# Performance work log

Measured on AMD Instinct MI355X. Metric: run time of the kernel, lower is better.

Reference implementation:

```python
import jax, jax.numpy as jnp
import numpy as np

B, S, HID = 2, 2048, 2048
NH = 16
HD = HID // NH  # 128


def setup_inputs() -> dict:
    key = jax.random.key(0)
    ks = jax.random.split(key, 9)
    w = 0.02  # init scale to keep logits in a sane range
    return {
        "hidden_states": jax.random.normal(ks[0], (B, S, HID), dtype=jnp.float32),
        "Wq": jax.random.normal(ks[1], (HID, HID), dtype=jnp.float32) * w,
        "bq": jnp.zeros((HID,), dtype=jnp.float32),
        "Wk": jax.random.normal(ks[2], (HID, HD), dtype=jnp.float32) * w,
        "bk": jnp.zeros((HD,), dtype=jnp.float32),
        "Wv": jax.random.normal(ks[3], (HID, HD), dtype=jnp.float32) * w,
        "bv": jnp.zeros((HD,), dtype=jnp.float32),
        "Wo": jax.random.normal(ks[4], (HID, HID), dtype=jnp.float32) * w,
        "bo": jnp.zeros((HID,), dtype=jnp.float32),
    }


def reference(hidden_states, Wq, bq, Wk, bk, Wv, bv, Wo, bo):
    b, s, _ = hidden_states.shape
    # Projections (weights stored [in, out])
    q = hidden_states @ Wq + bq                      # [B,S,HID]
    k = hidden_states @ Wk + bk                      # [B,S,HD] single shared KV head
    v = hidden_states @ Wv + bv                      # [B,S,HD]
    q = q.reshape(b, s, NH, HD)                      # [B,S,H,D]
    # MQA: all query heads attend to the same K/V
    scores = jnp.einsum("bshd,btd->bhst", q, k) / jnp.sqrt(jnp.float32(HD))  # [B,H,S,S]
    probs = jax.nn.softmax(scores, axis=-1)
    attn = jnp.einsum("bhst,btd->bshd", probs, v)    # [B,S,H,D]
    attn = attn.reshape(b, s, HID)
    return attn @ Wo + bo
```

## Files before the change

### kernel.cpp

```cpp
#include <hip/hip_runtime.h>
#include <math.h>

#define BB  2
#define SS  2048
#define HID 2048
#define NH  16
#define HD  128
#define MT  (BB * SS)
#define NC  (HID + 2 * HD)
#define QK_SCALE 0.12751744f

typedef unsigned short ushort_t;
typedef unsigned int uint_t;
typedef __bf16 bf16x8 __attribute__((ext_vector_type(8)));
typedef short short8 __attribute__((ext_vector_type(8)));
typedef float f32x4 __attribute__((ext_vector_type(4)));

__device__ __forceinline__ ushort_t f2bf(float x) {
    union { float f; uint_t u; } a; a.f = x;
    return (ushort_t)((a.u + 0x7FFFu + ((a.u >> 16) & 1u)) >> 16);
}
__device__ __forceinline__ ushort_t f2bf_fast(float x) {
    union { float f; uint_t u; } a; a.f = x;
    return (ushort_t)((a.u + 0x8000u) >> 16);
}

__device__ __forceinline__ int sw_addr(int r, int c) {
    return ((r >> 1) << 6) + ((((((r & 1) << 2) | c)) ^ ((r >> 1) & 7)) << 3);
}

#define CFENCE() asm volatile("" ::: "memory")

__global__ __launch_bounds__(256) void conv_bf16_kernel(
    const float* __restrict__ in, ushort_t* __restrict__ outb)
{
    const size_t i = ((size_t)blockIdx.x * 256 + threadIdx.x) * 8;
    const float4 a = *(const float4*)&in[i];
    const float4 b = *(const float4*)&in[i + 4];
    short8 o;
    o[0] = (short)f2bf(a.x); o[1] = (short)f2bf(a.y);
    o[2] = (short)f2bf(a.z); o[3] = (short)f2bf(a.w);
    o[4] = (short)f2bf(b.x); o[5] = (short)f2bf(b.y);
    o[6] = (short)f2bf(b.z); o[7] = (short)f2bf(b.w);
    *(short8*)&outb[i] = o;
}

__global__ __launch_bounds__(256) void convT_kernel(
    const float* __restrict__ W, ushort_t* __restrict__ Th, int K, int N)
{
    __shared__ float Ts[64][65];
    const int t = threadIdx.x;
    const int k0 = blockIdx.x * 64, n0 = blockIdx.y * 64;
    const int rr = t >> 4, c4 = (t & 15) * 4;
#pragma unroll
    for (int i = 0; i < 4; i++) {
        const int k = rr + i * 16;
        const float4 v = *(const float4*)&W[(size_t)(k0 + k) * N + n0 + c4];
        Ts[k][c4 + 0] = v.x; Ts[k][c4 + 1] = v.y;
        Ts[k][c4 + 2] = v.z; Ts[k][c4 + 3] = v.w;
    }
    __syncthreads();
    const int n = t >> 2, kc = (t & 3) * 16;
    short8 hv[2];
#pragma unroll
    for (int jj = 0; jj < 16; jj++)
        hv[jj >> 3][jj & 7] = (short)f2bf(Ts[kc + jj][n]);
    const size_t ob = (size_t)(n0 + n) * K + k0 + kc;
    *(short8*)&Th[ob]     = hv[0];
    *(short8*)&Th[ob + 8] = hv[1];
}

template<int GX, int MODE>
__global__ __launch_bounds__(512, 2) void gemm256_kernel(
    const ushort_t* __restrict__ Ab, const ushort_t* __restrict__ WT,
    const float* __restrict__ bqp, const float* __restrict__ bkp,
    const float* __restrict__ bvp,
    ushort_t* __restrict__ qb, ushort_t* __restrict__ kb,
    ushort_t* __restrict__ vtb, float* __restrict__ Cf)
{
    __shared__ short lds[32768];
    constexpr int K = HID;
    const int t = threadIdx.x;
    const int w = t >> 6, ln = t & 63;
    const int wm = w >> 2, wn = w & 3;
    const int nh = wn >> 1;
    const int q = ln >> 4, lm = ln & 15;

    const int nwg = GX * (MT / 256);
    const int bid = blockIdx.x;
    const int sw = (bid & 7) * (nwg >> 3) + (bid >> 3);
    const int bx = sw % GX, by = sw / GX;
    const int row0 = by * 256, col0 = bx * 256;

    const int lrow = w * 8 + (ln >> 3);
    const int sb = (ln & 7) ^ (lrow & 7);
    const int rs = lrow * 2 + (sb >> 2);
    const int cc = sb & 3;
    size_t agb[2], bgb[2];
    agb[0] = (size_t)(row0 + rs) * K + cc * 8;
    agb[1] = (size_t)(row0 + 128 + rs) * K + cc * 8;
    bgb[0] = (size_t)(col0 + rs) * K + cc * 8;
    bgb[1] = (size_t)(col0 + 128 + rs) * K + cc * 8;
    const int lseg = w * 512;

    int aofl[8], bofl[4];
#pragma unroll
    for (int mf = 0; mf < 8; mf++) aofl[mf] = sw_addr(mf * 16 + lm, q);
#pragma unroll
    for (int nf = 0; nf < 4; nf++) bofl[nf] = sw_addr((wn & 1) * 64 + nf * 16 + lm, q);

#define ACH(bufv, hv) ((((bufv) << 1) | (hv)) << 12)
#define STAGE_A(bufv, hv, kcol) \
    __builtin_amdgcn_global_load_lds( \
        (const __attribute__((address_space(1))) void*)(Ab + agb[hv] + (kcol)), \
        (__attribute__((address_space(3))) void*)&lds[ACH(bufv, hv) + lseg], 16, 0, 0)
#define STAGE_B(bufv, hv, kcol) \
    __builtin_amdgcn_global_load_lds( \
        (const __attribute__((address_space(1))) void*)(WT + bgb[hv] + (kcol)), \
        (__attribute__((address_space(3))) void*)&lds[16384 + ACH(bufv, hv) + lseg], 16, 0, 0)

    f32x4 acc[8][4];
#pragma unroll
    for (int i = 0; i < 8; i++)
#pragma unroll
        for (int j = 0; j < 4; j++) acc[i][j] = 0.f;

    STAGE_A(0, 0, 0); STAGE_A(0, 1, 0);
    STAGE_B(0, 0, 0); STAGE_B(0, 1, 0);

    for (int kt = 0; kt < K; kt += 32) {
        const int cur = (kt >> 5) & 1, nxt = cur ^ 1;
        const bool more = (kt + 32 < K);

        if (more) {
            STAGE_A(nxt, 0, kt + 32); STAGE_A(nxt, 1, kt + 32);
            STAGE_B(nxt, 0, kt + 32); STAGE_B(nxt, 1, kt + 32);
            asm volatile("s_waitcnt vmcnt(4)" ::: "memory");
        } else {
            asm volatile("s_waitcnt vmcnt(0)" ::: "memory");
        }
        CFENCE(); __builtin_amdgcn_s_barrier(); CFENCE();

        bf16x8 ah[8], bh[4];
#pragma unroll
        for (int mf = 0; mf < 8; mf++)
            ah[mf] = *(const bf16x8*)&lds[ACH(cur, wm) + aofl[mf]];
#pragma unroll
        for (int nf = 0; nf < 4; nf++)
            bh[nf] = *(const bf16x8*)&lds[16384 + ACH(cur, nh) + bofl[nf]];

        __builtin_amdgcn_s_setprio(1);
#pragma unroll
        for (int mf = 0; mf < 8; mf++)
#pragma unroll
            for (int nf = 0; nf < 4; nf++)
                acc[mf][nf] = __builtin_amdgcn_mfma_f32_16x16x32_bf16(
                    ah[mf], bh[nf], acc[mf][nf], 0, 0, 0);
        __builtin_amdgcn_s_setprio(0);

        CFENCE(); __builtin_amdgcn_s_barrier(); CFENCE();
    }
#undef STAGE_A
#undef STAGE_B
#undef ACH

#pragma unroll
    for (int nf = 0; nf < 4; nf++) {
        const int nnb = col0 + wn * 64 + nf * 16;
        const int nn = nnb + lm;
        if (MODE == 1) {
            const float bj = bqp[nn];
#pragma unroll
            for (int mf = 0; mf < 8; mf++) {
                const int mb = row0 + wm * 128 + mf * 16 + q * 4;
#pragma unroll
                for (int r = 0; r < 4; r++)
                    Cf[(size_t)(mb + r) * HID + nn] = acc[mf][nf][r] + bj;
            }
        } else {
            const int mode = (nnb < HID) ? 0 : ((nnb < HID + HD) ? 1 : 2);
            const float bj = (mode == 0) ? bqp[nn]
                           : (mode == 1) ? bkp[nn - HID] : bvp[nn - HID - HD];
#pragma unroll
            for (int mf = 0; mf < 8; mf++) {
                const int mb = row0 + wm * 128 + mf * 16 + q * 4;
#pragma unroll
                for (int r = 0; r < 4; r++) {
                    const float v = acc[mf][nf][r] + bj;
                    if (mode == 0)
                        qb[(size_t)(mb + r) * HID + nn] = f2bf_fast(v * QK_SCALE);
                    else if (mode == 1)
                        kb[(size_t)(mb + r) * HD + (nn - HID)] = f2bf_fast(v);
                    else
                        vtb[(size_t)(nn - HID - HD) * MT + (mb + r)] = f2bf_fast(v);
                }
            }
        }
    }
}

__global__ __launch_bounds__(128, 2) void attn_mfma_kernel(
    const ushort_t* __restrict__ qg, const ushort_t* __restrict__ kg,
    const ushort_t* __restrict__ vtg, ushort_t* Oh)
{
    __shared__ short Ks[8192], Vts[8192], Ps[4096];
    const int b = blockIdx.z, h = blockIdx.y, qt = blockIdx.x;
    const int t = threadIdx.x, wv = t >> 6, ln = t & 63;
    const int q = ln >> 4, lm = ln & 15;
    const int w32 = wv * 32;
    const int lm7 = ln & 7;

    const ushort_t* qgb = qg + (size_t)(b * SS + qt * 64) * HID + h * HD;
#pragma unroll
    for (int i = 0; i < 8; i++) {
        const int I = wv * 8 + i;
        const int r = 4 * I + (ln >> 4);
        const int c = (ln & 15) ^ (r & 15);
        __builtin_amdgcn_global_load_lds(
            (const __attribute__((address_space(1))) void*)(qgb + (size_t)r * HID + c * 8),
            (__attribute__((address_space(3))) void*)&Ks[I * 512], 16, 0, 0);
    }
    __syncthreads();
    bf16x8 aq[2][4];
#pragma unroll
    for (int st = 0; st < 2; st++) {
        const int am = w32 + st * 16 + lm;
#pragma unroll
        for (int ks = 0; ks < 4; ks++)
            aq[st][ks] = *(const bf16x8*)&Ks[am * 128 + (((ks << 2) | q) ^ (am & 15)) * 8];
    }
    __syncthreads();

    const ushort_t* kgb = kg + (size_t)b * SS * HD;
    const ushort_t* vgb = vtg + b * SS;
    uint_t koff[8], voff[8];
#pragma unroll
    for (int i = 0; i < 8; i++) {
        const int I = wv * 8 + i;
        { const int r = 4 * I + (ln >> 4); const int c = (ln & 15) ^ (r & 15);
          koff[i] = (uint_t)(r * HD + c * 8); }
        { const int r = 8 * I + (ln >> 3); const int c = (ln & 7) ^ (r & 7);
          voff[i] = (uint_t)(r * MT + c * 8); }
    }

#pragma unroll
    for (int i = 0; i < 8; i++) {
        const int I = wv * 8 + i;
        __builtin_amdgcn_global_load_lds(
            (const __attribute__((address_space(1))) void*)(kgb + koff[i]),
            (__attribute__((address_space(3))) void*)&Ks[I * 512], 16, 0, 0);
    }
#pragma unroll
    for (int i = 0; i < 8; i++) {
        const int I = wv * 8 + i;
        __builtin_amdgcn_global_load_lds(
            (const __attribute__((address_space(1))) void*)(vgb + voff[i]),
            (__attribute__((address_space(3))) void*)&Vts[I * 512], 16, 0, 0);
    }

    float lrow[2][4] = {{0.f, 0.f, 0.f, 0.f}, {0.f, 0.f, 0.f, 0.f}};
    f32x4 O[2][8];
#pragma unroll
    for (int st = 0; st < 2; st++)
#pragma unroll
        for (int ct = 0; ct < 8; ct++) O[st][ct] = 0.f;

    for (int kt = 0; kt < SS; kt += 64) {
        const int more = (kt + 64 < SS);

        asm volatile("s_waitcnt vmcnt(8)" ::: "memory");
        CFENCE();
        __builtin_amdgcn_s_barrier();
        CFENCE();

        f32x4 s[2][4];
#pragma unroll
        for (int st = 0; st < 2; st++)
#pragma unroll
            for (int ct = 0; ct < 4; ct++) s[st][ct] = 0.f;
        __builtin_amdgcn_s_setprio(1);
#pragma unroll
        for (int ks = 0; ks < 4; ks++) {
#pragma unroll
            for (int ct = 0; ct < 4; ct++) {
                const int n = ct * 16 + lm;
                const bf16x8 bk = *(const bf16x8*)&Ks[n * 128 + (((ks << 2) | q) ^ (n & 15)) * 8];
                s[0][ct] = __builtin_amdgcn_mfma_f32_16x16x32_bf16(aq[0][ks], bk, s[0][ct], 0, 0, 0);
                s[1][ct] = __builtin_amdgcn_mfma_f32_16x16x32_bf16(aq[1][ks], bk, s[1][ct], 0, 0, 0);
            }
        }
        __builtin_amdgcn_s_setprio(0);

        CFENCE();
        __builtin_amdgcn_s_barrier();
        CFENCE();
        if (more) {
#pragma unroll
            for (int i = 0; i < 8; i++) {
                const int I = wv * 8 + i;
                __builtin_amdgcn_global_load_lds(
                    (const __attribute__((address_space(1))) void*)(kgb + koff[i] + (kt + 64) * HD),
                    (__attribute__((address_space(3))) void*)&Ks[I * 512], 16, 0, 0);
            }
        }

#pragma unroll
        for (int st = 0; st < 2; st++)
#pragma unroll
        for (int ct = 0; ct < 4; ct++) {
            const int ch = ct * 2 + (lm >> 3);
#pragma unroll
            for (int r = 0; r < 4; r++) {
                const float p = exp2f(s[st][ct][r]);
                lrow[st][r] += p;
                const int pr = w32 + st * 16 + q * 4 + r;
                Ps[pr * 64 + ((ch ^ (pr & 7)) << 3) + lm7] = (short)f2bf_fast(p);
            }
        }

        if (more) asm volatile("s_waitcnt vmcnt(8)" ::: "memory");
        else      asm volatile("s_waitcnt vmcnt(0)" ::: "memory");
        CFENCE();
        __builtin_amdgcn_s_barrier();
        CFENCE();

        __builtin_amdgcn_s_setprio(1);
#pragma unroll
        for (int ks = 0; ks < 2; ks++) {
            const bf16x8 ap0 = *(const bf16x8*)&Ps[(w32 + lm) * 64 + (((ks << 2) | q) ^ lm7) * 8];
            const bf16x8 ap1 = *(const bf16x8*)&Ps[(w32 + 16 + lm) * 64 + (((ks << 2) | q) ^ lm7) * 8];
#pragma unroll
            for (int ct = 0; ct < 8; ct++) {
                const int d = ct * 16 + lm;
                const bf16x8 bv = *(const bf16x8*)&Vts[d * 64 + (((ks << 2) | q) ^ (d & 7)) * 8];
                O[0][ct] = __builtin_amdgcn_mfma_f32_16x16x32_bf16(ap0, bv, O[0][ct], 0, 0, 0);
                O[1][ct] = __builtin_amdgcn_mfma_f32_16x16x32_bf16(ap1, bv, O[1][ct], 0, 0, 0);
            }
        }
        __builtin_amdgcn_s_setprio(0);

        CFENCE();
        __builtin_amdgcn_s_barrier();
        CFENCE();
        if (more) {
#pragma unroll
            for (int i = 0; i < 8; i++) {
                const int I = wv * 8 + i;
                __builtin_amdgcn_global_load_lds(
                    (const __attribute__((address_space(1))) void*)(vgb + voff[i] + (kt + 64)),
                    (__attribute__((address_space(3))) void*)&Vts[I * 512], 16, 0, 0);
            }
        }
    }

#pragma unroll
    for (int msk = 1; msk < 16; msk <<= 1)
#pragma unroll
        for (int st = 0; st < 2; st++)
#pragma unroll
            for (int r = 0; r < 4; r++) lrow[st][r] += __shfl_xor(lrow[st][r], msk);
#pragma unroll
    for (int st = 0; st < 2; st++)
#pragma unroll
    for (int r = 0; r < 4; r++) {
        const float inv = 1.f / lrow[st][r];
        const size_t base = (size_t)(b * SS + qt * 64 + w32 + st * 16 + q * 4 + r) * HID + h * HD;
#pragma unroll
        for (int ct = 0; ct < 8; ct++)
            Oh[base + ct * 16 + lm] = f2bf_fast(O[st][ct][r] * inv);
    }
}

extern "C" void kernel_launch(void* const* d_in, const int* in_sizes, int n_in,
                              void* d_out, int out_size, void* d_ws, size_t ws_size,
                              hipStream_t stream)
{
    const float* hs = (const float*)d_in[0];
    const float* Wq = (const float*)d_in[1];
    const float* bq = (const float*)d_in[2];
    const float* Wk = (const float*)d_in[3];
    const float* bk = (const float*)d_in[4];
    const float* Wv = (const float*)d_in[5];
    const float* bv = (const float*)d_in[6];
    const float* Wo = (const float*)d_in[7];
    const float* bo = (const float*)d_in[8];
    float* out = (float*)d_out;

    char* w = (char*)d_ws;
    ushort_t* hsb  = (ushort_t*)w;  w += (size_t)MT * HID * 2;
    ushort_t* qb   = (ushort_t*)w;  w += (size_t)MT * HID * 2;
    ushort_t* kb   = (ushort_t*)w;  w += (size_t)MT * HD * 2;
    ushort_t* vtb  = (ushort_t*)w;  w += (size_t)HD * MT * 2;
    ushort_t* WcT  = (ushort_t*)w;  w += (size_t)NC * HID * 2;
    ushort_t* WoT  = WcT;

    conv_bf16_kernel<<<(MT * HID) / (256 * 8), 256, 0, stream>>>(hs, hsb);
    convT_kernel<<<dim3(HID / 64, HID / 64), 256, 0, stream>>>(Wq, WcT, HID, HID);
    convT_kernel<<<dim3(HID / 64, HD / 64),  256, 0, stream>>>(
        Wk, WcT + (size_t)HID * HID, HID, HD);
    convT_kernel<<<dim3(HID / 64, HD / 64),  256, 0, stream>>>(
        Wv, WcT + (size_t)(HID + HD) * HID, HID, HD);

    gemm256_kernel<NC / 256, 0><<<(NC / 256) * (MT / 256), 512, 0, stream>>>(
        hsb, WcT, bq, bk, bv, qb, kb, vtb, nullptr);

    convT_kernel<<<dim3(HID / 64, HID / 64), 256, 0, stream>>>(Wo, WoT, HID, HID);

    attn_mfma_kernel<<<dim3(SS / 64, NH, BB), 128, 0, stream>>>(qb, kb, vtb, qb);

    gemm256_kernel<HID / 256, 1><<<(HID / 256) * (MT / 256), 512, 0, stream>>>(
        qb, WoT, bo, nullptr, nullptr, nullptr, nullptr, nullptr, out);
}
```

Measured before the change: 359.5 us.

## Deepen GEMM K-step to 64 with interleaved staged loads across four MFMA phases

The projection GEMM kernel now processes K in 64-wide steps, doubling LDS to 128KB. Each step is split into four MFMA quadrant phases, and the next tile's global-to-LDS loads are issued chunk by chunk between them so copies overlap compute with fewer full waits per K. The attention softmax also swaps exp2f for the hardware exp2 builtin. Risks: the larger LDS footprint likely caps occupancy at one workgroup per CU despite launch_bounds(512,2), and there are more barriers per iteration.

```diff
diff --git a/kernel.cpp b/kernel.cpp
--- a/kernel.cpp
+++ b/kernel.cpp
@@ -78,7 +78,7 @@
     ushort_t* __restrict__ qb, ushort_t* __restrict__ kb,
     ushort_t* __restrict__ vtb, float* __restrict__ Cf)
 {
-    __shared__ short lds[32768];
+    __shared__ short lds[65536];
     constexpr int K = HID;
     const int t = threadIdx.x;
     const int w = t >> 6, ln = t & 63;
@@ -109,15 +109,15 @@
 #pragma unroll
     for (int nf = 0; nf < 4; nf++) bofl[nf] = sw_addr((wn & 1) * 64 + nf * 16 + lm, q);
 
-#define ACH(bufv, hv) ((((bufv) << 1) | (hv)) << 12)
-#define STAGE_A(bufv, hv, kcol) \
+#define CHUNK(bufv, hv, kcv) ((((bufv) << 2) | ((hv) << 1) | (kcv)) << 12)
+#define STAGE_A(bufv, hv, kcv, kcol) \
     __builtin_amdgcn_global_load_lds( \
-        (const __attribute__((address_space(1))) void*)(Ab + agb[hv] + (kcol)), \
-        (__attribute__((address_space(3))) void*)&lds[ACH(bufv, hv) + lseg], 16, 0, 0)
-#define STAGE_B(bufv, hv, kcol) \
+        (const __attribute__((address_space(1))) void*)(Ab + agb[hv] + (kcol) + (kcv) * 32), \
+        (__attribute__((address_space(3))) void*)&lds[CHUNK(bufv, hv, kcv) + lseg], 16, 0, 0)
+#define STAGE_B(bufv, hv, kcv, kcol) \
     __builtin_amdgcn_global_load_lds( \
-        (const __attribute__((address_space(1))) void*)(WT + bgb[hv] + (kcol)), \
-        (__attribute__((address_space(3))) void*)&lds[16384 + ACH(bufv, hv) + lseg], 16, 0, 0)
+        (const __attribute__((address_space(1))) void*)(WT + bgb[hv] + (kcol) + (kcv) * 32), \
+        (__attribute__((address_space(3))) void*)&lds[32768 + CHUNK(bufv, hv, kcv) + lseg], 16, 0, 0)
 
     f32x4 acc[8][4];
 #pragma unroll
@@ -125,44 +125,101 @@
 #pragma unroll
         for (int j = 0; j < 4; j++) acc[i][j] = 0.f;
 
-    STAGE_A(0, 0, 0); STAGE_A(0, 1, 0);
-    STAGE_B(0, 0, 0); STAGE_B(0, 1, 0);
-
-    for (int kt = 0; kt < K; kt += 32) {
-        const int cur = (kt >> 5) & 1, nxt = cur ^ 1;
-        const bool more = (kt + 32 < K);
+    STAGE_A(0, 0, 0, 0); STAGE_B(0, 0, 0, 0);
+    STAGE_A(0, 0, 1, 0); STAGE_B(0, 0, 1, 0);
+    STAGE_A(0, 1, 0, 0); STAGE_B(0, 1, 0, 0);
+    STAGE_A(0, 1, 1, 0); STAGE_B(0, 1, 1, 0);
+
+    for (int kt = 0; kt < K; kt += 64) {
+        const int cur = (kt >> 6) & 1, nxt = cur ^ 1;
+        const bool more = (kt + 64 < K);
+        const int kn = kt + 64;
+        bf16x8 ah[4][2], bh[4][2];
 
         if (more) {
-            STAGE_A(nxt, 0, kt + 32); STAGE_A(nxt, 1, kt + 32);
-            STAGE_B(nxt, 0, kt + 32); STAGE_B(nxt, 1, kt + 32);
-            asm volatile("s_waitcnt vmcnt(4)" ::: "memory");
+            STAGE_A(nxt, 0, 0, kn); STAGE_B(nxt, 0, 0, kn);
+            asm volatile("s_waitcnt vmcnt(2)" ::: "memory");
         } else {
             asm volatile("s_waitcnt vmcnt(0)" ::: "memory");
         }
         CFENCE(); __builtin_amdgcn_s_barrier(); CFENCE();
-
-        bf16x8 ah[8], bh[4];
-#pragma unroll
-        for (int mf = 0; mf < 8; mf++)
-            ah[mf] = *(const bf16x8*)&lds[ACH(cur, wm) + aofl[mf]];
-#pragma unroll
-        for (int nf = 0; nf < 4; nf++)
-            bh[nf] = *(const bf16x8*)&lds[16384 + ACH(cur, nh) + bofl[nf]];
-
-        __builtin_amdgcn_s_setprio(1);
-#pragma unroll
-        for (int mf = 0; mf < 8; mf++)
-#pragma unroll
-            for (int nf = 0; nf < 4; nf++)
-                acc[mf][nf] = __builtin_amdgcn_mfma_f32_16x16x32_bf16(
-                    ah[mf], bh[nf], acc[mf][nf], 0, 0, 0);
-        __builtin_amdgcn_s_setprio(0);
-
+#pragma unroll
+        for (int mfl = 0; mfl < 4; mfl++)
+#pragma unroll
+            for (int ks = 0; ks < 2; ks++)
+                ah[mfl][ks] = *(const bf16x8*)&lds[CHUNK(cur, wm, ks) + aofl[mfl]];
+#pragma unroll
+        for (int nfl = 0; nfl < 2; nfl++)
+#pragma unroll
+            for (int ks = 0; ks < 2; ks++)
+                bh[nfl][ks] = *(const bf16x8*)&lds[32768 + CHUNK(cur, nh, ks) + bofl[nfl]];
+        __builtin_amdgcn_s_setprio(1);
+#pragma unroll
+        for (int ks = 0; ks < 2; ks++)
+#pragma unroll
+            for (int mfl = 0; mfl < 4; mfl++)
+#pragma unroll
+                for (int nfl = 0; nfl < 2; nfl++)
+                    acc[mfl][nfl] = __builtin_amdgcn_mfma_f32_16x16x32_bf16(
+                        ah[mfl][ks], bh[nfl][ks], acc[mfl][nfl], 0, 0, 0);
+        __builtin_amdgcn_s_setprio(0);
+        CFENCE(); __builtin_amdgcn_s_barrier(); CFENCE();
+
+#pragma unroll
+        for (int nfl = 2; nfl < 4; nfl++)
+#pragma unroll
+            for (int ks = 0; ks < 2; ks++)
+                bh[nfl][ks] = *(const bf16x8*)&lds[32768 + CHUNK(cur, nh, ks) + bofl[nfl]];
+        if (more) { STAGE_A(nxt, 0, 1, kn); STAGE_B(nxt, 0, 1, kn); }
+        CFENCE(); __builtin_amdgcn_s_barrier(); CFENCE();
+        __builtin_amdgcn_s_setprio(1);
+#pragma unroll
+        for (int ks = 0; ks < 2; ks++)
+#pragma unroll
+            for (int mfl = 0; mfl < 4; mfl++)
+#pragma unroll
+            for (int nfl = 2; nfl < 4; nfl++)
+                acc[mfl][nfl] = __builtin_amdgcn_mfma_f32_16x16x32_bf16(
+                    ah[mfl][ks], bh[nfl][ks], acc[mfl][nfl], 0, 0, 0);
+        __builtin_amdgcn_s_setprio(0);
+        CFENCE(); __builtin_amdgcn_s_barrier(); CFENCE();
+
+#pragma unroll
+        for (int mfl = 0; mfl < 4; mfl++)
+#pragma unroll
+            for (int ks = 0; ks < 2; ks++)
+                ah[mfl][ks] = *(const bf16x8*)&lds[CHUNK(cur, wm, ks) + aofl[4 + mfl]];
+        if (more) { STAGE_A(nxt, 1, 0, kn); STAGE_B(nxt, 1, 0, kn); }
+        CFENCE(); __builtin_amdgcn_s_barrier(); CFENCE();
+        __builtin_amdgcn_s_setprio(1);
+#pragma unroll
+        for (int ks = 0; ks < 2; ks++)
+#pragma unroll
+            for (int mfl = 0; mfl < 4; mfl++)
+#pragma unroll
+            for (int nfl = 0; nfl < 2; nfl++)
+                acc[4 + mfl][nfl] = __builtin_amdgcn_mfma_f32_16x16x32_bf16(
+                    ah[mfl][ks], bh[nfl][ks], acc[4 + mfl][nfl], 0, 0, 0);
+        __builtin_amdgcn_s_setprio(0);
+        CFENCE(); __builtin_amdgcn_s_barrier(); CFENCE();
+
+        if (more) { STAGE_A(nxt, 1, 1, kn); STAGE_B(nxt, 1, 1, kn); }
+        CFENCE(); __builtin_amdgcn_s_barrier(); CFENCE();
+        __builtin_amdgcn_s_setprio(1);
+#pragma unroll
+        for (int ks = 0; ks < 2; ks++)
+#pragma unroll
+            for (int mfl = 0; mfl < 4; mfl++)
+#pragma unroll
+            for (int nfl = 2; nfl < 4; nfl++)
+                acc[4 + mfl][nfl] = __builtin_amdgcn_mfma_f32_16x16x32_bf16(
+                    ah[mfl][ks], bh[nfl][ks], acc[4 + mfl][nfl], 0, 0, 0);
+        __builtin_amdgcn_s_setprio(0);
         CFENCE(); __builtin_amdgcn_s_barrier(); CFENCE();
     }
 #undef STAGE_A
 #undef STAGE_B
-#undef ACH
+#undef CHUNK
 
 #pragma unroll
     for (int nf = 0; nf < 4; nf++) {
@@ -311,7 +368,7 @@
             const int ch = ct * 2 + (lm >> 3);
 #pragma unroll
             for (int r = 0; r < 4; r++) {
-                const float p = exp2f(s[st][ct][r]);
+                const float p = __builtin_amdgcn_exp2f(s[st][ct][r]);
                 lrow[st][r] += p;
                 const int pr = w32 + st * 16 + q * 4 + r;
                 Ps[pr * 64 + ((ch ^ (pr & 7)) << 3) + lm7] = (short)f2bf_fast(p);
```

After: 339.5 us. 1.06x faster.
